# Kernel optimization log

Measured on AMD Instinct MI355X. Metric: run time of the kernel, lower is better.

The kernel has to match this reference:

```python
import jax, jax.numpy as jnp
import numpy as np

B, N = 16, 4096

def _fps(xyz, npoint):
    # iterative farthest point sampling on one cloud [n,3] -> [npoint] int32
    n = xyz.shape[0]
    def body(carry, _):
        dist, far = carry
        d = jnp.sum((xyz - xyz[far]) ** 2, axis=-1)
        dist = jnp.minimum(dist, d)
        return (dist, jnp.argmax(dist).astype(jnp.int32)), far
    _, idx = jax.lax.scan(body, (jnp.full((n,), 1e10, jnp.float32), jnp.int32(0)), None, length=npoint)
    return idx

def _ball_query(radius, nsample, xyz, new_xyz):
    # xyz [n,3], new_xyz [S,3] -> [S,nsample] neighbor indices (first-in-index order, as in PointNet++)
    n = xyz.shape[0]
    sqr = jnp.sum((new_xyz[:, None, :] - xyz[None, :, :]) ** 2, axis=-1)  # [S,n]
    idx = jnp.where(sqr > radius * radius, n, jnp.arange(n, dtype=jnp.int32)[None, :])
    idx = jnp.sort(idx, axis=-1)[:, :nsample]
    return jnp.where(idx == n, idx[:, :1], idx)

def _gather(p, i):
    return jax.vmap(lambda pp, ii: pp[ii])(p, i)

def _mlp(x, layers):
    # shared MLP = 1x1 conv over grouped points; BN(eval) folded into (W,b)
    for W, b in layers:
        x = jax.nn.relu(jnp.einsum('bsnc,co->bsno', x, W) + b)
    return x

def _sa(xyz, feats, npoint, radius, nsample, layers):
    fps_idx = jax.vmap(lambda p: _fps(p, npoint))(xyz)            # [B,S]
    new_xyz = _gather(xyz, fps_idx)                                # [B,S,3]
    idx = jax.vmap(lambda p, q: _ball_query(radius, nsample, p, q))(xyz, new_xyz)  # [B,S,ns]
    x = _gather(xyz, idx) - new_xyz[:, :, None, :]                 # centered grouped xyz
    if feats is not None:
        x = jnp.concatenate([x, _gather(feats, idx)], axis=-1)
    x = _mlp(x, layers)
    return new_xyz, jnp.max(x, axis=2)

def _forward(points, w10, b10, w11, b11, w12, b12, w20, b20, w21, b21, w22, b22, w30, b30, w31, b31, w32, b32, lw1, lb1, lw2, lb2, fw1, fb1, fw2, fb2, pos_mean, pos_std, rot_mean, rot_std):
    l1x, l1f = _sa(points, None, 512, 0.2, 32, [(w10, b10), (w11, b11), (w12, b12)])
    l2x, l2f = _sa(l1x, l1f, 128, 0.4, 64, [(w20, b20), (w21, b21), (w22, b22)])
    # sa3: group_all
    x = jnp.concatenate([l2x, l2f], axis=-1)[:, None]              # [B,1,128,259]
    x = _mlp(x, [(w30, b30), (w31, b31), (w32, b32)])
    g = jnp.max(x, axis=2).reshape(points.shape[0], 1024)
    label = jax.nn.sigmoid(jax.nn.relu(g @ lw1 + lb1) @ lw2 + lb2)  # dropout = identity (eval)
    res = jax.nn.relu(g @ fw1 + fb1) @ fw2 + fb2
    pl = res[:, 0:3] * pos_std + pos_mean
    rl = res[:, 3:9] * rot_std + rot_mean
    pr = res[:, 9:12] * pos_std + pos_mean
    rr = res[:, 12:18] * rot_std + rot_mean
    return jnp.concatenate([label, pl, rl, pr, rr], axis=-1)       # [B,20]

def setup_inputs():
    ks = iter(jax.random.split(jax.random.key(0), 64))
    def w(shape, s=0.05):
        return jax.random.normal(next(ks), shape, jnp.float32) * s
    inp = {'points': jax.random.normal(next(ks), (B, N, 3), jnp.float32) * 0.5}
    dims = {'w10': (3, 64), 'w11': (64, 64), 'w12': (64, 128), 'w20': (131, 128), 'w21': (128, 128), 'w22': (128, 256), 'w30': (259, 256), 'w31': (256, 512), 'w32': (512, 1024), 'lw1': (1024, 256), 'lw2': (256, 2), 'fw1': (1024, 512), 'fw2': (512, 18)}
    for name, s in dims.items():
        inp[name] = w(s)
        inp[name.replace('w', 'b', 1)] = jnp.zeros((s[1],), jnp.float32)
    inp['pos_mean'] = w((3,), 0.1)
    inp['pos_std'] = jnp.abs(w((3,))) + 1.0
    inp['rot_mean'] = w((6,), 0.1)
    inp['rot_std'] = jnp.abs(w((6,))) + 1.0
    return inp

def reference(points, w10, b10, w11, b11, w12, b12, w20, b20, w21, b21, w22, b22, w30, b30, w31, b31, w32, b32, lw1, lb1, lw2, lb2, fw1, fb1, fw2, fb2, pos_mean, pos_std, rot_mean, rot_std):
    return _forward(points, w10, b10, w11, b11, w12, b12, w20, b20, w21, b21, w22, b22, w30, b30, w31, b31, w32, b32, lw1, lb1, lw2, lb2, fw1, fb1, fw2, fb2, pos_mean, pos_std, rot_mean, rot_std)
```

## Files before the change

### kernel.cpp

```cpp
#include <hip/hip_runtime.h>
#include <math.h>

#define BB 16
#define NN 4096

typedef float v2f __attribute__((ext_vector_type(2)));
typedef short bfrag8 __attribute__((ext_vector_type(8)));
typedef float fx4 __attribute__((ext_vector_type(4)));

__device__ __forceinline__ v2f pkfma(v2f a, v2f b, v2f c) {
    return __builtin_elementwise_fma(a, b, c);
}

__device__ __forceinline__ fx4 mfma16(bfrag8 a, bfrag8 b, fx4 c) {
    return __builtin_amdgcn_mfma_f32_16x16x32_bf16(a, b, c, 0, 0, 0);
}

__device__ __forceinline__ unsigned short bf16rne(float v) {
    unsigned u = __float_as_uint(v);
    return (unsigned short)((u + 0x7FFFu + ((u >> 16) & 1u)) >> 16);
}
__device__ __forceinline__ void bf16split(float v, unsigned short& h, unsigned short& l) {
    h = bf16rne(v);
    float fh = __uint_as_float((unsigned)h << 16);
    l = bf16rne(v - fh);
}

__device__ __forceinline__ float sq3(float dx, float dy, float dz) {
    return __fadd_rn(__fadd_rn(__fmul_rn(dx, dx), __fmul_rn(dy, dy)), __fmul_rn(dz, dz));
}

template<int CTRL, int RMASK>
__device__ __forceinline__ unsigned long long dpp_max_step(unsigned long long P) {
    int lo = __builtin_amdgcn_update_dpp(0, (int)(unsigned)P,        CTRL, RMASK, 0xf, true);
    int hi = __builtin_amdgcn_update_dpp(0, (int)(unsigned)(P >> 32), CTRL, RMASK, 0xf, true);
    unsigned long long o = ((unsigned long long)(unsigned)hi << 32) | (unsigned)lo;
    return (o > P) ? o : P;
}

__device__ __forceinline__ unsigned long long dpp_wave_max_u64(unsigned long long P) {
    P = dpp_max_step<0x111, 0xf>(P);
    P = dpp_max_step<0x112, 0xf>(P);
    P = dpp_max_step<0x114, 0xf>(P);
    P = dpp_max_step<0x118, 0xf>(P);
    P = dpp_max_step<0x142, 0xa>(P);
    P = dpp_max_step<0x143, 0xc>(P);
    return P;
}

__device__ __forceinline__ unsigned long long u64max(unsigned long long a, unsigned long long b) {
    return (a > b) ? a : b;
}

template<int NPTS, int NPOINT, int TPB>
__global__ __launch_bounds__(TPB) void fps_kernel(const float* __restrict__ xyz,
                                                  float* __restrict__ newxyz,
                                                  float* __restrict__ out_t,
                                                  int ts) {
    constexpr int PPT = NPTS / TPB;
    constexpr int NW  = TPB / 64;
    static_assert(NPOINT <= TPB, "far-history latch needs NPOINT <= TPB");
    __shared__ float sx[NPTS], sy[NPTS], sz[NPTS];
    __shared__ __align__(16) unsigned long long slot[2][NW];
    const int b = blockIdx.x;
    const int tid = threadIdx.x;
    const float* base = xyz + (size_t)b * NPTS * 3;
    for (int i = tid; i < NPTS; i += TPB) {
        sx[i] = base[i * 3 + 0];
        sy[i] = base[i * 3 + 1];
        sz[i] = base[i * 3 + 2];
    }
    __syncthreads();
    float px[PPT], py[PPT], pz[PPT], dist[PPT];
#pragma unroll
    for (int k = 0; k < PPT; k++) {
        int p = tid + k * TPB;
        px[k] = sx[p]; py[k] = sy[p]; pz[k] = sz[p];
        dist[k] = 1e10f;
    }
    int far = 0;
    int myfar = 0;
    const int lane = tid & 63, wid = tid >> 6;
    for (int it = 0; it < NPOINT; it++) {
        if (tid == it) myfar = far;
        float fx = sx[far], fy = sy[far], fz = sz[far];
        float bv = -1.0f; int bi = 0;
#pragma unroll
        for (int k = 0; k < PPT; k++) {
            float d = sq3(px[k] - fx, py[k] - fy, pz[k] - fz);
            float nd = fminf(dist[k], d);
            dist[k] = nd;
            if (nd > bv) { bv = nd; bi = tid + k * TPB; }
        }
        unsigned long long P = ((unsigned long long)__float_as_uint(bv) << 32)
                             | (unsigned long long)(~(unsigned)bi & 0xFFFFFFFFull);
        P = dpp_wave_max_u64(P);
        int bufi = it & 1;
        if (lane == 63) slot[bufi][wid] = P;
        __syncthreads();
        unsigned long long v[NW];
#pragma unroll
        for (int w = 0; w < NW; w++) v[w] = slot[bufi][w];
#pragma unroll
        for (int st = NW / 2; st >= 1; st >>= 1)
#pragma unroll
            for (int w = 0; w < st; w++) v[w] = u64max(v[w], v[w + st]);
        far = (int)(~(unsigned)(v[0] & 0xFFFFFFFFull));
    }
    if (tid < NPOINT) {
        float fx = sx[myfar], fy = sy[myfar], fz = sz[myfar];
        newxyz[((size_t)b * NPOINT + tid) * 3 + 0] = fx;
        newxyz[((size_t)b * NPOINT + tid) * 3 + 1] = fy;
        newxyz[((size_t)b * NPOINT + tid) * 3 + 2] = fz;
        if (out_t) {
            out_t[0 * ts + b * NPOINT + tid] = fx;
            out_t[1 * ts + b * NPOINT + tid] = fy;
            out_t[2 * ts + b * NPOINT + tid] = fz;
        }
    }
}

template<int NS>
__device__ __forceinline__ void bq_body(const float* __restrict__ pts, int n,
                                        const float* __restrict__ centers, int S,
                                        float r2, int* __restrict__ outidx,
                                        int wave, int lane) {
    int b = wave / S, s = wave % S;
    const float* c = centers + ((size_t)b * S + s) * 3;
    float cx = c[0], cy = c[1], cz = c[2];
    const float* pb = pts + (size_t)b * n * 3;
    int* out = outidx + ((size_t)b * S + s) * NS;
    int total = 0, first = -1;
    int rounds = n >> 6;
    for (int r = 0; r < rounds; r++) {
        int p = (r << 6) + lane;
        float dx = pb[p * 3 + 0] - cx, dy = pb[p * 3 + 1] - cy, dz = pb[p * 3 + 2] - cz;
        float d = sq3(dx, dy, dz);
        bool pred = (d <= r2);
        unsigned long long mask = __ballot(pred);
        if (first < 0 && mask) first = (r << 6) + (__ffsll(mask) - 1);
        if (pred) {
            int rank = total + __popcll(mask & ((1ull << lane) - 1ull));
            if (rank < NS) out[rank] = p;
        }
        total += __popcll(mask);
        if (total >= NS) break;
    }
    for (int j = total + lane; j < NS; j += 64) out[j] = first;
}

__global__ __launch_bounds__(512) void bq1_fps2_kernel(const float* __restrict__ points,
                                                       const float* __restrict__ l1x,
                                                       float* __restrict__ l2x,
                                                       float* __restrict__ x3t,
                                                       int* __restrict__ idx1,
                                                       float r2a,
                                                       const float* __restrict__ w21,
                                                       const float* __restrict__ w22,
                                                       const float* __restrict__ w11s,
                                                       const float* __restrict__ w12s,
                                                       float* __restrict__ w21f,
                                                       float* __restrict__ w22f,
                                                       float* __restrict__ w11f,
                                                       float* __restrict__ w12f) {
    __shared__ float sx[512], sy[512], sz[512];
    const int tid = threadIdx.x;
    const int lane = tid & 63, wid = tid >> 6;
    if (blockIdx.x < 16) {
        if (wid != 0) return;
        const int b = blockIdx.x;
        const float* base = l1x + (size_t)b * 512 * 3;
        for (int i = lane; i < 512; i += 64) {
            sx[i] = base[i * 3 + 0];
            sy[i] = base[i * 3 + 1];
            sz[i] = base[i * 3 + 2];
        }
        float px[8], py[8], pz[8], dist[8];
#pragma unroll
        for (int k = 0; k < 8; k++) {
            int p = lane + k * 64;
            px[k] = sx[p]; py[k] = sy[p]; pz[k] = sz[p];
            dist[k] = 1e10f;
        }
        int far = 0, myfar0 = 0, myfar1 = 0;
        for (int it = 0; it < 128; it++) {
            if (lane == it) myfar0 = far;
            if (lane == it - 64) myfar1 = far;
            float fx = sx[far], fy = sy[far], fz = sz[far];
            float bv = -1.0f; int bi = 0;
#pragma unroll
            for (int k = 0; k < 8; k++) {
                float d = sq3(px[k] - fx, py[k] - fy, pz[k] - fz);
                float nd = fminf(dist[k], d);
                dist[k] = nd;
                if (nd > bv) { bv = nd; bi = lane + k * 64; }
            }
            unsigned long long P = ((unsigned long long)__float_as_uint(bv) << 32)
                                 | (unsigned long long)(~(unsigned)bi & 0xFFFFFFFFull);
            P = dpp_wave_max_u64(P);
            unsigned lo = (unsigned)__builtin_amdgcn_readlane((int)(unsigned)P, 63);
            far = (int)(~lo);
        }
        {
            int s0 = lane, s1 = lane + 64;
            float a = sx[myfar0], c1 = sy[myfar0], c2 = sz[myfar0];
            l2x[((size_t)b * 128 + s0) * 3 + 0] = a;
            l2x[((size_t)b * 128 + s0) * 3 + 1] = c1;
            l2x[((size_t)b * 128 + s0) * 3 + 2] = c2;
            x3t[0 * 2048 + b * 128 + s0] = a;
            x3t[1 * 2048 + b * 128 + s0] = c1;
            x3t[2 * 2048 + b * 128 + s0] = c2;
            float d = sx[myfar1], e = sy[myfar1], f = sz[myfar1];
            l2x[((size_t)b * 128 + s1) * 3 + 0] = d;
            l2x[((size_t)b * 128 + s1) * 3 + 1] = e;
            l2x[((size_t)b * 128 + s1) * 3 + 2] = f;
            x3t[0 * 2048 + b * 128 + s1] = d;
            x3t[1 * 2048 + b * 128 + s1] = e;
            x3t[2 * 2048 + b * 128 + s1] = f;
        }
    } else if (blockIdx.x < 1040) {
        int wave = (blockIdx.x - 16) * 8 + wid;
        bq_body<32>(points, 4096, l1x, 512, r2a, idx1, wave, lane);
    } else {
        int gt = (blockIdx.x - 1040) * 512 + tid;
        const float* W; float* OF; int NT, KT, N; int t;
        if (gt < 4096)       { W = w21;  OF = w21f; NT = 8;  KT = 4; N = 128; t = gt; }
        else if (gt < 12288) { W = w22;  OF = w22f; NT = 16; KT = 4; N = 256; t = gt - 4096; }
        else if (gt < 13312) { W = w11s; OF = w11f; NT = 4;  KT = 2; N = 64;  t = gt - 12288; }
        else                 { W = w12s; OF = w12f; NT = 8;  KT = 2; N = 128; t = gt - 13312; }
        int L = t & 63;
        int rest = t >> 6;
        int nt = rest & (NT - 1);
        int hk = rest / NT;
        int kt = hk % KT, hl = hk / KT;
        int k0 = kt * 32 + (L >> 4) * 8;
        int n  = nt * 16 + (L & 15);
        unsigned o[4];
#pragma unroll
        for (int e = 0; e < 4; e++) {
            float va = W[(size_t)(k0 + 2 * e + 0) * N + n];
            float vb = W[(size_t)(k0 + 2 * e + 1) * N + n];
            unsigned short ha, la, hb, lb;
            bf16split(va, ha, la);
            bf16split(vb, hb, lb);
            o[e] = hl ? ((unsigned)la | ((unsigned)lb << 16))
                      : ((unsigned)ha | ((unsigned)hb << 16));
        }
        ((uint4*)OF)[t] = make_uint4(o[0], o[1], o[2], o[3]);
    }
}

__global__ __launch_bounds__(64, 2) void sa1_bq2_kernel(const float* __restrict__ xyz, const float* __restrict__ l1x,
                                                 const int* __restrict__ idx1,
                                                 const float* __restrict__ l2x, int* __restrict__ idx2, float r2b,
                                                 const float* __restrict__ W1, const float* __restrict__ B1,
                                                 const float* __restrict__ W2f, const float* __restrict__ B2,
                                                 const float* __restrict__ W3f, const float* __restrict__ B3,
                                                 float* __restrict__ l1f) {
    __shared__ short hsh[64 * 72];
    __shared__ short hsl[64 * 72];
    int lane = threadIdx.x;
    if (blockIdx.x < 2048) {
        bq_body<64>(l1x, 512, l2x, 128, r2b, idx2, blockIdx.x, lane);
        return;
    }
    int blk = blockIdx.x - 2048;
    int b = blk >> 8;
    int ct = lane >> 5, nn = lane & 31;
    int s = ((blk & 255) << 1) | ct;
    int center = b * 512 + s;
    int c0 = b * 512 + ((blk & 255) << 1);
    int ii = idx1[center * 32 + nn];
    float px = xyz[((size_t)b * NN + ii) * 3 + 0] - l1x[(size_t)center * 3 + 0];
    float py = xyz[((size_t)b * NN + ii) * 3 + 1] - l1x[(size_t)center * 3 + 1];
    float pz = xyz[((size_t)b * NN + ii) * 3 + 2] - l1x[(size_t)center * 3 + 2];
#pragma unroll
    for (int c2 = 0; c2 < 32; c2++) {
        int ca = 2 * c2, cb = 2 * c2 + 1;
        float v0 = fmaxf(B1[ca] + px * W1[ca] + py * W1[64 + ca] + pz * W1[128 + ca], 0.0f);
        float v1 = fmaxf(B1[cb] + px * W1[cb] + py * W1[64 + cb] + pz * W1[128 + cb], 0.0f);
        unsigned short h0, l0, h1, l1;
        bf16split(v0, h0, l0);
        bf16split(v1, h1, l1);
        int base = lane * 72 + ca;
        *(unsigned*)(&hsh[base]) = (unsigned)h0 | ((unsigned)h1 << 16);
        *(unsigned*)(&hsl[base]) = (unsigned)l0 | ((unsigned)l1 << 16);
    }
    __syncthreads();
    {
        fx4 acc[4][4];
#pragma unroll
        for (int mt = 0; mt < 4; mt++)
#pragma unroll
            for (int nt = 0; nt < 4; nt++) {
                float bn = B2[nt * 16 + (lane & 15)];
                acc[mt][nt] = (fx4){bn, bn, bn, bn};
            }
        const bfrag8* w2v = (const bfrag8*)W2f;
#pragma unroll
        for (int kt = 0; kt < 2; kt++) {
            bfrag8 ah[4], al[4];
#pragma unroll
            for (int mt = 0; mt < 4; mt++) {
                int idx = (mt * 16 + (lane & 15)) * 72 + kt * 32 + (lane >> 4) * 8;
                ah[mt] = *(const bfrag8*)(&hsh[idx]);
                al[mt] = *(const bfrag8*)(&hsl[idx]);
            }
#pragma unroll
            for (int nt = 0; nt < 4; nt++) {
                bfrag8 bh = w2v[(size_t)((0 + kt) * 4 + nt) * 64 + lane];
                bfrag8 bl = w2v[(size_t)((2 + kt) * 4 + nt) * 64 + lane];
#pragma unroll
                for (int mt = 0; mt < 4; mt++) {
                    acc[mt][nt] = mfma16(ah[mt], bh, acc[mt][nt]);
                    acc[mt][nt] = mfma16(ah[mt], bl, acc[mt][nt]);
                    acc[mt][nt] = mfma16(al[mt], bh, acc[mt][nt]);
                }
            }
        }
        __syncthreads();
#pragma unroll
        for (int mt = 0; mt < 4; mt++)
#pragma unroll
            for (int nt = 0; nt < 4; nt++)
#pragma unroll
                for (int r = 0; r < 4; r++) {
                    float v = fmaxf(acc[mt][nt][r], 0.0f);
                    int m = mt * 16 + (lane >> 4) * 4 + r;
                    int n = nt * 16 + (lane & 15);
                    unsigned short hb, lb;
                    bf16split(v, hb, lb);
                    hsh[m * 72 + n] = (short)hb;
                    hsl[m * 72 + n] = (short)lb;
                }
        __syncthreads();
    }
    const bfrag8* w3v = (const bfrag8*)W3f;
#pragma unroll 1
    for (int pass = 0; pass < 2; pass++) {
        int nbase = pass * 4;
        fx4 acc[4][4];
#pragma unroll
        for (int mt = 0; mt < 4; mt++)
#pragma unroll
            for (int nt = 0; nt < 4; nt++) {
                float bn = B3[(nbase + nt) * 16 + (lane & 15)];
                acc[mt][nt] = (fx4){bn, bn, bn, bn};
            }
#pragma unroll
        for (int kt = 0; kt < 2; kt++) {
            bfrag8 ah[4], al[4];
#pragma unroll
            for (int mt = 0; mt < 4; mt++) {
                int idx = (mt * 16 + (lane & 15)) * 72 + kt * 32 + (lane >> 4) * 8;
                ah[mt] = *(const bfrag8*)(&hsh[idx]);
                al[mt] = *(const bfrag8*)(&hsl[idx]);
            }
#pragma unroll
            for (int nt = 0; nt < 4; nt++) {
                bfrag8 bh = w3v[(size_t)((0 + kt) * 8 + nbase + nt) * 64 + lane];
                bfrag8 bl = w3v[(size_t)((2 + kt) * 8 + nbase + nt) * 64 + lane];
#pragma unroll
                for (int mt = 0; mt < 4; mt++) {
                    acc[mt][nt] = mfma16(ah[mt], bh, acc[mt][nt]);
                    acc[mt][nt] = mfma16(ah[mt], bl, acc[mt][nt]);
                    acc[mt][nt] = mfma16(al[mt], bh, acc[mt][nt]);
                }
            }
        }
#pragma unroll
        for (int nt = 0; nt < 4; nt++) {
            float mv0 = 0.0f, mv1 = 0.0f;
#pragma unroll
            for (int r = 0; r < 4; r++) {
                mv0 = fmaxf(mv0, fmaxf(acc[0][nt][r], acc[1][nt][r]));
                mv1 = fmaxf(mv1, fmaxf(acc[2][nt][r], acc[3][nt][r]));
            }
            mv0 = fmaxf(mv0, __shfl_xor(mv0, 16));
            mv0 = fmaxf(mv0, __shfl_xor(mv0, 32));
            mv1 = fmaxf(mv1, __shfl_xor(mv1, 16));
            mv1 = fmaxf(mv1, __shfl_xor(mv1, 32));
            int n = (nbase + nt) * 16 + (lane & 15);
            if (lane < 16)      l1f[(size_t)c0 * 128 + n] = mv0;
            else if (lane < 32) l1f[(size_t)(c0 + 1) * 128 + n] = mv1;
        }
    }
}

__global__ __launch_bounds__(256, 4) void sa2_kernel(const float* __restrict__ l1x, const float* __restrict__ l2x,
                                                  const float* __restrict__ l1f, const int* __restrict__ idx2,
                                                  const float* __restrict__ W1, const float* __restrict__ B1,
                                                  const float* __restrict__ w21f, const float* __restrict__ B2,
                                                  const float* __restrict__ w22f, const float* __restrict__ B3,
                                                  float* __restrict__ x3t) {
    __shared__ short hsh[64 * 136];
    __shared__ short hsl[64 * 136];
    int tid = threadIdx.x;
    int w = __builtin_amdgcn_readfirstlane(tid >> 6);
    int lane = tid & 63;
    int b = blockIdx.x >> 7, s = blockIdx.x & 127;
    int center = b * 128 + s;
    int ii = idx2[center * 64 + lane];
    float cx = l2x[(size_t)center * 3 + 0], cy = l2x[(size_t)center * 3 + 1], cz = l2x[(size_t)center * 3 + 2];
    const float* pr = l1x + ((size_t)b * 512 + ii) * 3;
    float px = pr[0] - cx, py = pr[1] - cy, pz = pr[2] - cz;
    const float4* frow = (const float4*)(l1f + ((size_t)b * 512 + ii) * 128);
    v2f h[16];
    {
        const v2f* B1v = (const v2f*)(B1 + w * 32);
        const v2f* w1a = (const v2f*)(W1 + 0 * 128 + w * 32);
        const v2f* w1b = (const v2f*)(W1 + 1 * 128 + w * 32);
        const v2f* w1c = (const v2f*)(W1 + 2 * 128 + w * 32);
        v2f px2 = {px, px}, py2 = {py, py}, pz2 = {pz, pz};
#pragma unroll
        for (int j = 0; j < 16; j++)
            h[j] = pkfma(pz2, w1c[j], pkfma(py2, w1b[j], pkfma(px2, w1a[j], B1v[j])));
    }
#pragma unroll 2
    for (int k4 = 0; k4 < 32; k4++) {
        float4 f = frow[k4];
        const v2f* wr = (const v2f*)(W1 + (3 + k4 * 4) * 128 + w * 32);
        v2f fx2 = {f.x, f.x}, fy2 = {f.y, f.y}, fz2 = {f.z, f.z}, fw2 = {f.w, f.w};
#pragma unroll
        for (int j = 0; j < 16; j++) {
            h[j] = pkfma(fx2, wr[j], h[j]);
            h[j] = pkfma(fy2, wr[64 + j], h[j]);
            h[j] = pkfma(fz2, wr[128 + j], h[j]);
            h[j] = pkfma(fw2, wr[192 + j], h[j]);
        }
    }
#pragma unroll
    for (int j = 0; j < 16; j++) {
        float v0 = fmaxf(h[j].x, 0.0f);
        float v1 = fmaxf(h[j].y, 0.0f);
        unsigned short h0, l0, h1, l1;
        bf16split(v0, h0, l0);
        bf16split(v1, h1, l1);
        int cb = lane * 136 + w * 32 + 2 * j;
        *(unsigned*)(&hsh[cb]) = (unsigned)h0 | ((unsigned)h1 << 16);
        *(unsigned*)(&hsl[cb]) = (unsigned)l0 | ((unsigned)l1 << 16);
    }
    __syncthreads();
    {
        fx4 acc[4][2];
#pragma unroll
        for (int mt = 0; mt < 4; mt++)
#pragma unroll
            for (int nt = 0; nt < 2; nt++) {
                float bn = B2[(2 * w + nt) * 16 + (lane & 15)];
                acc[mt][nt] = (fx4){bn, bn, bn, bn};
            }
#pragma unroll
        for (int kt = 0; kt < 4; kt++) {
            bfrag8 ah[4], al[4];
#pragma unroll
            for (int mt = 0; mt < 4; mt++) {
                int idx = (mt * 16 + (lane & 15)) * 136 + kt * 32 + (lane >> 4) * 8;
                ah[mt] = *(const bfrag8*)(&hsh[idx]);
                al[mt] = *(const bfrag8*)(&hsl[idx]);
            }
#pragma unroll
            for (int nt = 0; nt < 2; nt++) {
                int ng = 2 * w + nt;
                bfrag8 bh = ((const bfrag8*)w21f)[(size_t)((0 + kt) * 8 + ng) * 64 + lane];
                bfrag8 bl = ((const bfrag8*)w21f)[(size_t)((4 + kt) * 8 + ng) * 64 + lane];
#pragma unroll
                for (int mt = 0; mt < 4; mt++) {
                    acc[mt][nt] = mfma16(ah[mt], bh, acc[mt][nt]);
                    acc[mt][nt] = mfma16(ah[mt], bl, acc[mt][nt]);
                    acc[mt][nt] = mfma16(al[mt], bh, acc[mt][nt]);
                }
            }
        }
        __syncthreads();
#pragma unroll
        for (int mt = 0; mt < 4; mt++)
#pragma unroll
            for (int nt = 0; nt < 2; nt++)
#pragma unroll
                for (int r = 0; r < 4; r++) {
                    float v = fmaxf(acc[mt][nt][r], 0.0f);
                    int m = mt * 16 + (lane >> 4) * 4 + r;
                    int n = (2 * w + nt) * 16 + (lane & 15);
                    unsigned short hb, lb;
                    bf16split(v, hb, lb);
                    hsh[m * 136 + n] = (short)hb;
                    hsl[m * 136 + n] = (short)lb;
                }
        __syncthreads();
    }
#pragma unroll 1
    for (int pass = 0; pass < 2; pass++) {
        int nb = w * 4 + pass * 2;
        fx4 acc[4][2];
#pragma unroll
        for (int mt = 0; mt < 4; mt++)
#pragma unroll
            for (int nt = 0; nt < 2; nt++) {
                float bn = B3[(nb + nt) * 16 + (lane & 15)];
                acc[mt][nt] = (fx4){bn, bn, bn, bn};
            }
#pragma unroll
        for (int kt = 0; kt < 4; kt++) {
            bfrag8 ah[4], al[4];
#pragma unroll
            for (int mt = 0; mt < 4; mt++) {
                int idx = (mt * 16 + (lane & 15)) * 136 + kt * 32 + (lane >> 4) * 8;
                ah[mt] = *(const bfrag8*)(&hsh[idx]);
                al[mt] = *(const bfrag8*)(&hsl[idx]);
            }
#pragma unroll
            for (int nt = 0; nt < 2; nt++) {
                bfrag8 bh = ((const bfrag8*)w22f)[(size_t)((0 + kt) * 16 + (nb + nt)) * 64 + lane];
                bfrag8 bl = ((const bfrag8*)w22f)[(size_t)((4 + kt) * 16 + (nb + nt)) * 64 + lane];
#pragma unroll
                for (int mt = 0; mt < 4; mt++) {
                    acc[mt][nt] = mfma16(ah[mt], bh, acc[mt][nt]);
                    acc[mt][nt] = mfma16(ah[mt], bl, acc[mt][nt]);
                    acc[mt][nt] = mfma16(al[mt], bh, acc[mt][nt]);
                }
            }
        }
#pragma unroll
        for (int nt = 0; nt < 2; nt++) {
            float mv = 0.0f;
#pragma unroll
            for (int mt = 0; mt < 4; mt++)
#pragma unroll
                for (int r = 0; r < 4; r++)
                    mv = fmaxf(mv, acc[mt][nt][r]);
            mv = fmaxf(mv, __shfl_xor(mv, 16));
            mv = fmaxf(mv, __shfl_xor(mv, 32));
            if (lane < 16)
                x3t[(size_t)(3 + (nb + nt) * 16 + lane) * 2048 + center] = mv;
        }
    }
}

template<int K, int COUT, int CPT, bool MAXOUT>
__device__ __forceinline__ void gemm_t_body(const float* __restrict__ in_t,
                                            const float* __restrict__ W,
                                            const float* __restrict__ bias,
                                            float* __restrict__ outp,
                                            int bid, int lane) {
    int rw = bid & 31, cg = bid >> 5;
    int row = rw * 64 + lane;
    int cbase = cg * CPT;
    v2f acc[CPT / 2];
    const v2f* bv = (const v2f*)(bias + cbase);
#pragma unroll
    for (int j = 0; j < CPT / 2; j++) acc[j] = bv[j];
    for (int k = 0; k < K; k++) {
        float xk = in_t[(size_t)k * 2048 + row];
        v2f xk2 = {xk, xk};
        const v2f* wr = (const v2f*)(W + (size_t)k * COUT + cbase);
#pragma unroll
        for (int j = 0; j < CPT / 2; j++) acc[j] = pkfma(xk2, wr[j], acc[j]);
    }
    if (MAXOUT) {
        int b = row >> 7;
#pragma unroll
        for (int j = 0; j < CPT / 2; j++) {
            float va = fmaxf(acc[j].x, 0.0f);
            float vb = fmaxf(acc[j].y, 0.0f);
#pragma unroll
            for (int m = 32; m >= 1; m >>= 1) {
                va = fmaxf(va, __shfl_xor(va, m));
                vb = fmaxf(vb, __shfl_xor(vb, m));
            }
            if (lane == 0) {
                atomicMax((int*)(outp + (size_t)b * 1024 + cbase + 2 * j + 0), __float_as_int(va));
                atomicMax((int*)(outp + (size_t)b * 1024 + cbase + 2 * j + 1), __float_as_int(vb));
            }
        }
    } else {
#pragma unroll
        for (int j = 0; j < CPT / 2; j++) {
            outp[(size_t)(cbase + 2 * j + 0) * 2048 + row] = fmaxf(acc[j].x, 0.0f);
            outp[(size_t)(cbase + 2 * j + 1) * 2048 + row] = fmaxf(acc[j].y, 0.0f);
        }
    }
}

template<int K, int COUT, int CPT, bool MAXOUT>
__global__ __launch_bounds__(64, 4) void gemm_t_kernel(const float* __restrict__ in_t,
                                                    const float* __restrict__ W,
                                                    const float* __restrict__ bias,
                                                    float* __restrict__ outp) {
    gemm_t_body<K, COUT, CPT, MAXOUT>(in_t, W, bias, outp, blockIdx.x, threadIdx.x);
}

__global__ __launch_bounds__(64, 4) void gemm1_zerog_kernel(const float* __restrict__ in_t,
                                                            const float* __restrict__ W,
                                                            const float* __restrict__ bias,
                                                            float* __restrict__ outp,
                                                            float* __restrict__ g) {
    if (blockIdx.x < 1024) {
        gemm_t_body<259, 256, 8, false>(in_t, W, bias, outp, blockIdx.x, threadIdx.x);
    } else {
        g[(blockIdx.x - 1024) * 64 + threadIdx.x] = 0.0f;
    }
}

__global__ __launch_bounds__(512) void head_kernel(const float* __restrict__ g,
                                                   const float* __restrict__ lw1, const float* __restrict__ lb1,
                                                   const float* __restrict__ lw2, const float* __restrict__ lb2,
                                                   const float* __restrict__ fw1, const float* __restrict__ fb1,
                                                   const float* __restrict__ fw2, const float* __restrict__ fb2,
                                                   const float* __restrict__ pm, const float* __restrict__ ps,
                                                   const float* __restrict__ rm, const float* __restrict__ rs,
                                                   float* __restrict__ out) {
    __shared__ float gl[1024], a1[256], f1[512];
    int b = blockIdx.x, t = threadIdx.x;
    for (int i = t; i < 1024; i += 512) gl[i] = g[b * 1024 + i];
    __syncthreads();
    {
        float acc = fb1[t];
        for (int k = 0; k < 1024; k++) acc += gl[k] * fw1[k * 512 + t];
        f1[t] = fmaxf(acc, 0.0f);
    }
    if (t < 256) {
        float acc = lb1[t];
        for (int k = 0; k < 1024; k++) acc += gl[k] * lw1[k * 256 + t];
        a1[t] = fmaxf(acc, 0.0f);
    }
    __syncthreads();
    if (t < 2) {
        float z = lb2[t];
        for (int k = 0; k < 256; k++) z += a1[k] * lw2[k * 2 + t];
        out[b * 20 + t] = 1.0f / (1.0f + expf(-z));
    } else if (t < 20) {
        int i = t - 2;
        float z = fb2[i];
        for (int k = 0; k < 512; k++) z += f1[k] * fw2[k * 18 + i];
        float sc, mn;
        if (i < 3)       { sc = ps[i];      mn = pm[i]; }
        else if (i < 9)  { sc = rs[i - 3];  mn = rm[i - 3]; }
        else if (i < 12) { sc = ps[i - 9];  mn = pm[i - 9]; }
        else             { sc = rs[i - 12]; mn = rm[i - 12]; }
        out[b * 20 + t] = z * sc + mn;
    }
}

static inline size_t align256(size_t x) { return (x + 255) & ~(size_t)255; }

extern "C" void kernel_launch(void* const* d_in, const int* in_sizes, int n_in,
                              void* d_out, int out_size, void* d_ws, size_t ws_size,
                              hipStream_t stream) {
    const float* points = (const float*)d_in[0];
    const float* w10 = (const float*)d_in[1];  const float* b10 = (const float*)d_in[2];
    const float* w11 = (const float*)d_in[3];  const float* b11 = (const float*)d_in[4];
    const float* w12 = (const float*)d_in[5];  const float* b12 = (const float*)d_in[6];
    const float* w20 = (const float*)d_in[7];  const float* b20 = (const float*)d_in[8];
    const float* w21 = (const float*)d_in[9];  const float* b21 = (const float*)d_in[10];
    const float* w22 = (const float*)d_in[11]; const float* b22 = (const float*)d_in[12];
    const float* w30 = (const float*)d_in[13]; const float* b30 = (const float*)d_in[14];
    const float* w31 = (const float*)d_in[15]; const float* b31 = (const float*)d_in[16];
    const float* w32 = (const float*)d_in[17]; const float* b32 = (const float*)d_in[18];
    const float* lw1 = (const float*)d_in[19]; const float* lb1 = (const float*)d_in[20];
    const float* lw2 = (const float*)d_in[21]; const float* lb2 = (const float*)d_in[22];
    const float* fw1 = (const float*)d_in[23]; const float* fb1 = (const float*)d_in[24];
    const float* fw2 = (const float*)d_in[25]; const float* fb2 = (const float*)d_in[26];
    const float* pm  = (const float*)d_in[27]; const float* ps  = (const float*)d_in[28];
    const float* rm  = (const float*)d_in[29]; const float* rs  = (const float*)d_in[30];
    float* out = (float*)d_out;

    char* p = (char*)d_ws;
    float* l1x  = (float*)p; p += align256((size_t)BB * 512 * 3 * 4);
    int*   idx1 = (int*)p;   p += align256((size_t)BB * 512 * 32 * 4);
    float* l1f  = (float*)p; p += align256((size_t)BB * 512 * 128 * 4);
    float* l2x  = (float*)p; p += align256((size_t)BB * 128 * 3 * 4);
    int*   idx2 = (int*)p;   p += align256((size_t)BB * 128 * 64 * 4);
    float* x3t  = (float*)p; p += align256((size_t)259 * 2048 * 4);
    float* h1t  = (float*)p; p += align256((size_t)256 * 2048 * 4);
    float* h2t  = (float*)p; p += align256((size_t)512 * 2048 * 4);
    float* g    = (float*)p; p += align256((size_t)BB * 1024 * 4);
    float* w21f = h1t;
    float* w22f = h1t + (size_t)16384;
    float* w11f = h1t + (size_t)16384 + 32768;
    float* w12f = h1t + (size_t)16384 + 32768 + 4096;

    const float R2A = (float)(0.2 * 0.2);
    const float R2B = (float)(0.4 * 0.4);

    fps_kernel<4096, 512, 512><<<BB, 512, 0, stream>>>(points, l1x, (float*)nullptr, 0);
    bq1_fps2_kernel<<<1070, 512, 0, stream>>>(points, l1x, l2x, x3t, idx1, R2A,
                                              w21, w22, w11, w12, w21f, w22f, w11f, w12f);
    sa1_bq2_kernel<<<6144, 64, 0, stream>>>(points, l1x, idx1, l2x, idx2, R2B,
                                            w10, b10, w11f, b11, w12f, b12, l1f);
    sa2_kernel<<<2048, 256, 0, stream>>>(l1x, l2x, l1f, idx2, w20, b20, w21f, b21, w22f, b22, x3t);
    gemm1_zerog_kernel<<<1280, 64, 0, stream>>>(x3t, w30, b30, h1t, g);
    gemm_t_kernel<256, 512, 8, false><<<2048, 64, 0, stream>>>(h1t, w31, b31, h2t);
    gemm_t_kernel<512, 1024, 8, true><<<4096, 64, 0, stream>>>(h2t, w32, b32, g);
    head_kernel<<<BB, 512, 0, stream>>>(g, lw1, lb1, lw2, lb2, fw1, fb1, fw2, fb2, pm, ps, rm, rs, out);
}
```

Baseline: 821.8 us.

## Move SA2 first layer feature GEMM from packed FMA to split-bf16 MFMA

The first SA2 MLP layer (131->128) previously ran as per-lane packed fp32 FMAs over 128 features. Now the gathered neighbor features are split into bf16 hi/lo pairs in shared memory, the xyz part is applied with scalar FMAs, and the feature part runs as 3-term split-bf16 MFMA using weights pre-packed by the prep blocks of bq1_fps2. This aims to cut VALU work in sa2 but adds extra shared-memory round trips, syncs, prep blocks and a small precision change from the split-bf16 scheme.

Result: faster. 787.3 us (-4.2%).

```diff
diff --git a/kernel.cpp b/kernel.cpp
--- a/kernel.cpp
+++ b/kernel.cpp
@@ -159,10 +159,12 @@
                                                        const float* __restrict__ w22,
                                                        const float* __restrict__ w11s,
                                                        const float* __restrict__ w12s,
+                                                       const float* __restrict__ w20s,
                                                        float* __restrict__ w21f,
                                                        float* __restrict__ w22f,
                                                        float* __restrict__ w11f,
-                                                       float* __restrict__ w12f) {
+                                                       float* __restrict__ w12f,
+                                                       float* __restrict__ w20f) {
     __shared__ float sx[512], sy[512], sz[512];
     const int tid = threadIdx.x;
     const int lane = tid & 63, wid = tid >> 6;
@@ -224,10 +226,11 @@
     } else {
         int gt = (blockIdx.x - 1040) * 512 + tid;
         const float* W; float* OF; int NT, KT, N; int t;
-        if (gt < 4096)       { W = w21;  OF = w21f; NT = 8;  KT = 4; N = 128; t = gt; }
-        else if (gt < 12288) { W = w22;  OF = w22f; NT = 16; KT = 4; N = 256; t = gt - 4096; }
-        else if (gt < 13312) { W = w11s; OF = w11f; NT = 4;  KT = 2; N = 64;  t = gt - 12288; }
-        else                 { W = w12s; OF = w12f; NT = 8;  KT = 2; N = 128; t = gt - 13312; }
+        if (gt < 4096)       { W = w21;        OF = w21f; NT = 8;  KT = 4; N = 128; t = gt; }
+        else if (gt < 12288) { W = w22;        OF = w22f; NT = 16; KT = 4; N = 256; t = gt - 4096; }
+        else if (gt < 13312) { W = w11s;       OF = w11f; NT = 4;  KT = 2; N = 64;  t = gt - 12288; }
+        else if (gt < 15360) { W = w12s;       OF = w12f; NT = 8;  KT = 2; N = 128; t = gt - 13312; }
+        else                 { W = w20s + 384; OF = w20f; NT = 8;  KT = 4; N = 128; t = gt - 15360; }
         int L = t & 63;
         int rest = t >> 6;
         int nt = rest & (NT - 1);
@@ -390,11 +393,13 @@
 __global__ __launch_bounds__(256, 4) void sa2_kernel(const float* __restrict__ l1x, const float* __restrict__ l2x,
                                                   const float* __restrict__ l1f, const int* __restrict__ idx2,
                                                   const float* __restrict__ W1, const float* __restrict__ B1,
+                                                  const float* __restrict__ w20f,
                                                   const float* __restrict__ w21f, const float* __restrict__ B2,
                                                   const float* __restrict__ w22f, const float* __restrict__ B3,
                                                   float* __restrict__ x3t) {
     __shared__ short hsh[64 * 136];
     __shared__ short hsl[64 * 136];
+    __shared__ float sxyz[64 * 4];
     int tid = threadIdx.x;
     int w = __builtin_amdgcn_readfirstlane(tid >> 6);
     int lane = tid & 63;
@@ -404,43 +409,89 @@
     float cx = l2x[(size_t)center * 3 + 0], cy = l2x[(size_t)center * 3 + 1], cz = l2x[(size_t)center * 3 + 2];
     const float* pr = l1x + ((size_t)b * 512 + ii) * 3;
     float px = pr[0] - cx, py = pr[1] - cy, pz = pr[2] - cz;
-    const float4* frow = (const float4*)(l1f + ((size_t)b * 512 + ii) * 128);
-    v2f h[16];
+    if (w == 0) {
+        sxyz[lane * 4 + 0] = px;
+        sxyz[lane * 4 + 1] = py;
+        sxyz[lane * 4 + 2] = pz;
+    }
     {
-        const v2f* B1v = (const v2f*)(B1 + w * 32);
-        const v2f* w1a = (const v2f*)(W1 + 0 * 128 + w * 32);
-        const v2f* w1b = (const v2f*)(W1 + 1 * 128 + w * 32);
-        const v2f* w1c = (const v2f*)(W1 + 2 * 128 + w * 32);
-        v2f px2 = {px, px}, py2 = {py, py}, pz2 = {pz, pz};
-#pragma unroll
-        for (int j = 0; j < 16; j++)
-            h[j] = pkfma(pz2, w1c[j], pkfma(py2, w1b[j], pkfma(px2, w1a[j], B1v[j])));
-    }
-#pragma unroll 2
-    for (int k4 = 0; k4 < 32; k4++) {
-        float4 f = frow[k4];
-        const v2f* wr = (const v2f*)(W1 + (3 + k4 * 4) * 128 + w * 32);
-        v2f fx2 = {f.x, f.x}, fy2 = {f.y, f.y}, fz2 = {f.z, f.z}, fw2 = {f.w, f.w};
-#pragma unroll
-        for (int j = 0; j < 16; j++) {
-            h[j] = pkfma(fx2, wr[j], h[j]);
-            h[j] = pkfma(fy2, wr[64 + j], h[j]);
-            h[j] = pkfma(fz2, wr[128 + j], h[j]);
-            h[j] = pkfma(fw2, wr[192 + j], h[j]);
-        }
-    }
-#pragma unroll
-    for (int j = 0; j < 16; j++) {
-        float v0 = fmaxf(h[j].x, 0.0f);
-        float v1 = fmaxf(h[j].y, 0.0f);
-        unsigned short h0, l0, h1, l1;
-        bf16split(v0, h0, l0);
-        bf16split(v1, h1, l1);
-        int cb = lane * 136 + w * 32 + 2 * j;
-        *(unsigned*)(&hsh[cb]) = (unsigned)h0 | ((unsigned)h1 << 16);
-        *(unsigned*)(&hsl[cb]) = (unsigned)l0 | ((unsigned)l1 << 16);
+        const float4* frow = (const float4*)(l1f + ((size_t)b * 512 + ii) * 128);
+#pragma unroll
+        for (int j = 0; j < 8; j++) {
+            float4 f = frow[w * 8 + j];
+            unsigned short h0, l0, h1, l1, h2, l2, h3, l3;
+            bf16split(f.x, h0, l0);
+            bf16split(f.y, h1, l1);
+            bf16split(f.z, h2, l2);
+            bf16split(f.w, h3, l3);
+            int cb = lane * 136 + w * 32 + 4 * j;
+            *(unsigned*)(&hsh[cb + 0]) = (unsigned)h0 | ((unsigned)h1 << 16);
+            *(unsigned*)(&hsh[cb + 2]) = (unsigned)h2 | ((unsigned)h3 << 16);
+            *(unsigned*)(&hsl[cb + 0]) = (unsigned)l0 | ((unsigned)l1 << 16);
+            *(unsigned*)(&hsl[cb + 2]) = (unsigned)l2 | ((unsigned)l3 << 16);
+        }
     }
     __syncthreads();
+    {
+        fx4 acc[4][2];
+        float w0n[2], w1n[2], w2n[2];
+#pragma unroll
+        for (int nt = 0; nt < 2; nt++) {
+            int n = (2 * w + nt) * 16 + (lane & 15);
+            float bn = B1[n];
+            acc[0][nt] = (fx4){bn, bn, bn, bn};
+            acc[1][nt] = acc[0][nt]; acc[2][nt] = acc[0][nt]; acc[3][nt] = acc[0][nt];
+            w0n[nt] = W1[n]; w1n[nt] = W1[128 + n]; w2n[nt] = W1[256 + n];
+        }
+#pragma unroll
+        for (int mt = 0; mt < 4; mt++)
+#pragma unroll
+            for (int r = 0; r < 4; r++) {
+                int m = mt * 16 + (lane >> 4) * 4 + r;
+                float mx = sxyz[m * 4 + 0], my = sxyz[m * 4 + 1], mz = sxyz[m * 4 + 2];
+#pragma unroll
+                for (int nt = 0; nt < 2; nt++)
+                    acc[mt][nt][r] += mx * w0n[nt] + my * w1n[nt] + mz * w2n[nt];
+            }
+#pragma unroll
+        for (int kt = 0; kt < 4; kt++) {
+            bfrag8 ah[4], al[4];
+#pragma unroll
+            for (int mt = 0; mt < 4; mt++) {
+                int idx = (mt * 16 + (lane & 15)) * 136 + kt * 32 + (lane >> 4) * 8;
+                ah[mt] = *(const bfrag8*)(&hsh[idx]);
+                al[mt] = *(const bfrag8*)(&hsl[idx]);
+            }
+#pragma unroll
+            for (int nt = 0; nt < 2; nt++) {
+                int ng = 2 * w + nt;
+                bfrag8 bh = ((const bfrag8*)w20f)[(size_t)((0 + kt) * 8 + ng) * 64 + lane];
+                bfrag8 bl = ((const bfrag8*)w20f)[(size_t)((4 + kt) * 8 + ng) * 64 + lane];
+#pragma unroll
+                for (int mt = 0; mt < 4; mt++) {
+                    acc[mt][nt] = mfma16(ah[mt], bh, acc[mt][nt]);
+                    acc[mt][nt] = mfma16(ah[mt], bl, acc[mt][nt]);
+                    acc[mt][nt] = mfma16(al[mt], bh, acc[mt][nt]);
+                }
+            }
+        }
+        __syncthreads();
+#pragma unroll
+        for (int mt = 0; mt < 4; mt++)
+#pragma unroll
+            for (int nt = 0; nt < 2; nt++)
+#pragma unroll
+                for (int r = 0; r < 4; r++) {
+                    float v = fmaxf(acc[mt][nt][r], 0.0f);
+                    int m = mt * 16 + (lane >> 4) * 4 + r;
+                    int n = (2 * w + nt) * 16 + (lane & 15);
+                    unsigned short hb, lb;
+                    bf16split(v, hb, lb);
+                    hsh[m * 136 + n] = (short)hb;
+                    hsl[m * 136 + n] = (short)lb;
+                }
+        __syncthreads();
+    }
     {
         fx4 acc[4][2];
 #pragma unroll
@@ -677,18 +728,21 @@
     float* g    = (float*)p; p += align256((size_t)BB * 1024 * 4);
     float* w21f = h1t;
     float* w22f = h1t + (size_t)16384;
-    float* w11f = h1t + (size_t)16384 + 32768;
-    float* w12f = h1t + (size_t)16384 + 32768 + 4096;
+    float* w11f = h1t + (size_t)49152;
+    float* w12f = h1t + (size_t)53248;
+    float* w20f = h1t + (size_t)61440;
 
     const float R2A = (float)(0.2 * 0.2);
     const float R2B = (float)(0.4 * 0.4);
 
     fps_kernel<4096, 512, 512><<<BB, 512, 0, stream>>>(points, l1x, (float*)nullptr, 0);
-    bq1_fps2_kernel<<<1070, 512, 0, stream>>>(points, l1x, l2x, x3t, idx1, R2A,
-                                              w21, w22, w11, w12, w21f, w22f, w11f, w12f);
+    bq1_fps2_kernel<<<1078, 512, 0, stream>>>(points, l1x, l2x, x3t, idx1, R2A,
+                                              w21, w22, w11, w12, w20,
+                                              w21f, w22f, w11f, w12f, w20f);
     sa1_bq2_kernel<<<6144, 64, 0, stream>>>(points, l1x, idx1, l2x, idx2, R2B,
                                             w10, b10, w11f, b11, w12f, b12, l1f);
-    sa2_kernel<<<2048, 256, 0, stream>>>(l1x, l2x, l1f, idx2, w20, b20, w21f, b21, w22f, b22, x3t);
+    sa2_kernel<<<2048, 256, 0, stream>>>(l1x, l2x, l1f, idx2, w20, b20,
+                                         w20f, w21f, b21, w22f, b22, x3t);
     gemm1_zerog_kernel<<<1280, 64, 0, stream>>>(x3t, w30, b30, h1t, g);
     gemm_t_kernel<256, 512, 8, false><<<2048, 64, 0, stream>>>(h1t, w31, b31, h2t);
     gemm_t_kernel<512, 1024, 8, true><<<4096, 64, 0, stream>>>(h2t, w32, b32, g);
```
